# Performance work log

Measured on AMD Instinct MI355X. Metric: run time of the kernel, lower is better.

## Reference

```python
import jax, jax.numpy as jnp
import numpy as np

EPS = 1e-8


def setup_inputs() -> dict:
    key = jax.random.key(0)
    k1, k2 = jax.random.split(key)
    predict_pc = jax.random.normal(k1, (4, 3, 4096), dtype=jnp.float32)  # Bx3xM
    gt_pc = jax.random.normal(k2, (4, 3, 4096), dtype=jnp.float32)      # Bx3xN
    return {"predict_pc": predict_pc, "gt_pc": gt_pc}


def reference(predict_pc, gt_pc):
    # predict_pc: Bx3xM, gt_pc: Bx3xN ; k=1 nearest neighbor each direction
    p = jnp.transpose(predict_pc, (0, 2, 1))  # B,M,3
    g = jnp.transpose(gt_pc, (0, 2, 1))       # B,N,3
    p2 = jnp.sum(p * p, axis=-1)  # B,M
    g2 = jnp.sum(g * g, axis=-1)  # B,N
    # squared L2 pairwise distances, B,M,N (computed once, used both directions)
    d2 = p2[:, :, None] + g2[:, None, :] - 2.0 * jnp.einsum("bmd,bnd->bmn", p, g)
    idx_g = jnp.argmin(d2, axis=2)  # B,M : nearest gt for each predicted point
    idx_p = jnp.argmin(d2, axis=1)  # B,N : nearest predicted for each gt point
    nearest_g = jnp.take_along_axis(g, idx_g[:, :, None], axis=1)  # B,M,3
    nearest_p = jnp.take_along_axis(p, idx_p[:, :, None], axis=1)  # B,N,3
    # robust_norm: sqrt(sum over coord dim + 1e-8)
    fwd_elem = jnp.sqrt(jnp.sum((nearest_g - p) ** 2, axis=-1) + EPS)  # B,M
    bwd_elem = jnp.sqrt(jnp.sum((nearest_p - g) ** 2, axis=-1) + EPS)  # B,N
    return fwd_elem.mean() + bwd_elem.mean()
```

## Files before the change

kernel.cpp:

```cpp
#include <hip/hip_runtime.h>
#include <math.h>

#define BATCH 4
#define NPTS 4096
#define THREADS 256
#define P 4
#define SEGS 16
#define CSEG (NPTS / SEGS)
#define PTGRPS (NPTS / (THREADS * P))
#define PASS1_BLOCKS (2 * BATCH * PTGRPS * SEGS)
#define TOTAL_PTS (2 * BATCH * NPTS)
#define PASS2_BLOCKS 32

#define EPS 1e-8f
#define BIG 1e30f

#define PMIN_FLOATS (SEGS * TOTAL_PTS)

__global__ __launch_bounds__(THREADS) void chamfer_pass1(
    const float* __restrict__ pred, const float* __restrict__ gt,
    float* __restrict__ pmin)
{
    __shared__ float lx[CSEG], ly[CSEG], lz[CSEG];

    const int bid   = blockIdx.x;
    const int seg   = bid & (SEGS - 1);
    const int ptgrp = (bid >> 4) & (PTGRPS - 1);
    const int batch = (bid >> 6) & (BATCH - 1);
    const int dir   = bid >> 8;

    const float* pts  = (dir == 0) ? pred : gt;
    const float* cand = (dir == 0) ? gt   : pred;

    {
        const float* cb = cand + (size_t)batch * 3 * NPTS + seg * CSEG;
        const int t = threadIdx.x;
        lx[t] = cb[t];
        ly[t] = cb[NPTS + t];
        lz[t] = cb[2 * NPTS + t];
    }
    __syncthreads();

    const float* pb = pts + (size_t)batch * 3 * NPTS;
    const int pbase = ptgrp * (THREADS * P) + threadIdx.x;
    float px[P], py[P], pz[P], m[P];
    #pragma unroll
    for (int k = 0; k < P; ++k) {
        const int i = pbase + k * THREADS;
        px[k] = pb[i];
        py[k] = pb[NPTS + i];
        pz[k] = pb[2 * NPTS + i];
        m[k] = BIG;
    }

    const float4* lx4 = (const float4*)lx;
    const float4* ly4 = (const float4*)ly;
    const float4* lz4 = (const float4*)lz;

    #pragma unroll 2
    for (int g = 0; g < CSEG / 4; ++g) {
        const float4 X = lx4[g];
        const float4 Y = ly4[g];
        const float4 Z = lz4[g];
        #pragma unroll
        for (int k = 0; k < P; ++k) {
            float dx, dy, dz, d0, d1, d2, d3;
            dx = px[k] - X.x; dy = py[k] - Y.x; dz = pz[k] - Z.x;
            d0 = fmaf(dx, dx, fmaf(dy, dy, dz * dz));
            dx = px[k] - X.y; dy = py[k] - Y.y; dz = pz[k] - Z.y;
            d1 = fmaf(dx, dx, fmaf(dy, dy, dz * dz));
            dx = px[k] - X.z; dy = py[k] - Y.z; dz = pz[k] - Z.z;
            d2 = fmaf(dx, dx, fmaf(dy, dy, dz * dz));
            dx = px[k] - X.w; dy = py[k] - Y.w; dz = pz[k] - Z.w;
            d3 = fmaf(dx, dx, fmaf(dy, dy, dz * dz));
            m[k] = fminf(m[k], fminf(fminf(d0, d1), fminf(d2, d3)));
        }
    }

    const int gp = dir * (BATCH * NPTS) + batch * NPTS + pbase;
    #pragma unroll
    for (int k = 0; k < P; ++k)
        pmin[(size_t)seg * TOTAL_PTS + gp + k * THREADS] = m[k];
}

__global__ __launch_bounds__(THREADS) void chamfer_pass2(
    const float* __restrict__ pmin, float* __restrict__ bsum)
{
    const int pbase = blockIdx.x * (THREADS * P) + threadIdx.x;
    float acc = 0.0f;
    #pragma unroll
    for (int k = 0; k < P; ++k) {
        const int p = pbase + k * THREADS;
        float v = BIG;
        #pragma unroll
        for (int s = 0; s < SEGS; ++s)
            v = fminf(v, pmin[(size_t)s * TOTAL_PTS + p]);
        acc += sqrtf(v + EPS);
    }
    #pragma unroll
    for (int off = 32; off; off >>= 1) acc += __shfl_down(acc, off, 64);
    __shared__ float wsum[THREADS / 64];
    if ((threadIdx.x & 63) == 0) wsum[threadIdx.x >> 6] = acc;
    __syncthreads();
    if (threadIdx.x == 0)
        bsum[blockIdx.x] = (wsum[0] + wsum[1]) + (wsum[2] + wsum[3]);
}

__global__ void chamfer_pass3(const float* __restrict__ bsum, float* __restrict__ out)
{
    float v = (threadIdx.x < PASS2_BLOCKS) ? bsum[threadIdx.x] : 0.0f;
    #pragma unroll
    for (int off = 32; off; off >>= 1) v += __shfl_down(v, off, 64);
    if (threadIdx.x == 0)
        out[0] = v * (1.0f / (float)(BATCH * NPTS));
}

extern "C" void kernel_launch(void* const* d_in, const int* in_sizes, int n_in,
                              void* d_out, int out_size, void* d_ws, size_t ws_size,
                              hipStream_t stream) {
    const float* pred = (const float*)d_in[0];
    const float* gt   = (const float*)d_in[1];
    float* out  = (float*)d_out;
    float* pmin = (float*)d_ws;
    float* bsum = pmin + PMIN_FLOATS;

    chamfer_pass1<<<PASS1_BLOCKS, THREADS, 0, stream>>>(pred, gt, pmin);
    chamfer_pass2<<<PASS2_BLOCKS, THREADS, 0, stream>>>(pmin, bsum);
    chamfer_pass3<<<1, 64, 0, stream>>>(bsum, out);
}
```

Before: 77.40 us.

## Use dot-product expansion for nearest-neighbor search with packed float4 candidates

The pairwise search now uses the expansion |p-c|^2 = |p|^2 - 2(p·c - |c|^2/2). It precomputes -|c|^2/2 per candidate and packs (x,y,z,s) into one float4 in shared memory, so each pair costs three FMAs plus a max instead of subtracts, squares and a min. It also doubles points per thread to 8 and candidate segments to 32, which halves candidate tile size and doubles the partial-min buffer that pass 2 reduces. The expanded form can suffer cancellation and go slightly negative, so pass 2 clamps at zero. Larger per-thread work and the bigger intermediate buffer trade occupancy and memory traffic for less ALU work.

```diff
diff --git a/kernel.cpp b/kernel.cpp
--- a/kernel.cpp
+++ b/kernel.cpp
@@ -4,13 +4,14 @@
 #define BATCH 4
 #define NPTS 4096
 #define THREADS 256
-#define P 4
-#define SEGS 16
+#define P 8
+#define SEGS 32
 #define CSEG (NPTS / SEGS)
 #define PTGRPS (NPTS / (THREADS * P))
 #define PASS1_BLOCKS (2 * BATCH * PTGRPS * SEGS)
 #define TOTAL_PTS (2 * BATCH * NPTS)
 #define PASS2_BLOCKS 32
+#define P2 (TOTAL_PTS / (PASS2_BLOCKS * THREADS))
 
 #define EPS 1e-8f
 #define BIG 1e30f
@@ -21,81 +22,78 @@
     const float* __restrict__ pred, const float* __restrict__ gt,
     float* __restrict__ pmin)
 {
-    __shared__ float lx[CSEG], ly[CSEG], lz[CSEG];
+    __shared__ float4 lc[CSEG];
 
     const int bid   = blockIdx.x;
     const int seg   = bid & (SEGS - 1);
-    const int ptgrp = (bid >> 4) & (PTGRPS - 1);
+    const int ptgrp = (bid >> 5) & (PTGRPS - 1);
     const int batch = (bid >> 6) & (BATCH - 1);
     const int dir   = bid >> 8;
 
     const float* pts  = (dir == 0) ? pred : gt;
     const float* cand = (dir == 0) ? gt   : pred;
 
-    {
+    if (threadIdx.x < CSEG) {
         const float* cb = cand + (size_t)batch * 3 * NPTS + seg * CSEG;
-        const int t = threadIdx.x;
-        lx[t] = cb[t];
-        ly[t] = cb[NPTS + t];
-        lz[t] = cb[2 * NPTS + t];
+        const float x = cb[threadIdx.x];
+        const float y = cb[NPTS + threadIdx.x];
+        const float z = cb[2 * NPTS + threadIdx.x];
+        const float s = -0.5f * fmaf(x, x, fmaf(y, y, z * z));
+        lc[threadIdx.x] = make_float4(x, y, z, s);
     }
     __syncthreads();
 
     const float* pb = pts + (size_t)batch * 3 * NPTS;
     const int pbase = ptgrp * (THREADS * P) + threadIdx.x;
-    float px[P], py[P], pz[P], m[P];
+    float px[P], py[P], pz[P], smax[P];
     #pragma unroll
     for (int k = 0; k < P; ++k) {
         const int i = pbase + k * THREADS;
         px[k] = pb[i];
         py[k] = pb[NPTS + i];
         pz[k] = pb[2 * NPTS + i];
-        m[k] = BIG;
+        smax[k] = -BIG;
     }
-
-    const float4* lx4 = (const float4*)lx;
-    const float4* ly4 = (const float4*)ly;
-    const float4* lz4 = (const float4*)lz;
 
     #pragma unroll 2
     for (int g = 0; g < CSEG / 4; ++g) {
-        const float4 X = lx4[g];
-        const float4 Y = ly4[g];
-        const float4 Z = lz4[g];
+        const float4 c0 = lc[4 * g + 0];
+        const float4 c1 = lc[4 * g + 1];
+        const float4 c2 = lc[4 * g + 2];
+        const float4 c3 = lc[4 * g + 3];
         #pragma unroll
         for (int k = 0; k < P; ++k) {
-            float dx, dy, dz, d0, d1, d2, d3;
-            dx = px[k] - X.x; dy = py[k] - Y.x; dz = pz[k] - Z.x;
-            d0 = fmaf(dx, dx, fmaf(dy, dy, dz * dz));
-            dx = px[k] - X.y; dy = py[k] - Y.y; dz = pz[k] - Z.y;
-            d1 = fmaf(dx, dx, fmaf(dy, dy, dz * dz));
-            dx = px[k] - X.z; dy = py[k] - Y.z; dz = pz[k] - Z.z;
-            d2 = fmaf(dx, dx, fmaf(dy, dy, dz * dz));
-            dx = px[k] - X.w; dy = py[k] - Y.w; dz = pz[k] - Z.w;
-            d3 = fmaf(dx, dx, fmaf(dy, dy, dz * dz));
-            m[k] = fminf(m[k], fminf(fminf(d0, d1), fminf(d2, d3)));
+            float t0 = fmaf(px[k], c0.x, fmaf(py[k], c0.y, fmaf(pz[k], c0.z, c0.w)));
+            float t1 = fmaf(px[k], c1.x, fmaf(py[k], c1.y, fmaf(pz[k], c1.z, c1.w)));
+            float t2 = fmaf(px[k], c2.x, fmaf(py[k], c2.y, fmaf(pz[k], c2.z, c2.w)));
+            float t3 = fmaf(px[k], c3.x, fmaf(py[k], c3.y, fmaf(pz[k], c3.z, c3.w)));
+            smax[k] = fmaxf(smax[k], fmaxf(fmaxf(t0, t1), fmaxf(t2, t3)));
         }
     }
 
     const int gp = dir * (BATCH * NPTS) + batch * NPTS + pbase;
     #pragma unroll
-    for (int k = 0; k < P; ++k)
-        pmin[(size_t)seg * TOTAL_PTS + gp + k * THREADS] = m[k];
+    for (int k = 0; k < P; ++k) {
+        const int i = pbase + k * THREADS;
+        const float p2 = fmaf(px[k], px[k], fmaf(py[k], py[k], pz[k] * pz[k]));
+        (void)i;
+        pmin[(size_t)seg * TOTAL_PTS + gp + k * THREADS] = fmaf(-2.0f, smax[k], p2);
+    }
 }
 
 __global__ __launch_bounds__(THREADS) void chamfer_pass2(
     const float* __restrict__ pmin, float* __restrict__ bsum)
 {
-    const int pbase = blockIdx.x * (THREADS * P) + threadIdx.x;
+    const int pbase = blockIdx.x * (THREADS * P2) + threadIdx.x;
     float acc = 0.0f;
     #pragma unroll
-    for (int k = 0; k < P; ++k) {
+    for (int k = 0; k < P2; ++k) {
         const int p = pbase + k * THREADS;
         float v = BIG;
         #pragma unroll
         for (int s = 0; s < SEGS; ++s)
             v = fminf(v, pmin[(size_t)s * TOTAL_PTS + p]);
-        acc += sqrtf(v + EPS);
+        acc += sqrtf(fmaxf(v, 0.0f) + EPS);
     }
     #pragma unroll
     for (int off = 32; off; off >>= 1) acc += __shfl_down(acc, off, 64);
```

Result: faster. 71.47 us (-7.7%).
